# Performance work log

Hardware: AMD Instinct MI355X
Metric: run time of the kernel (lower is better)

## Reference

```python
import jax, jax.numpy as jnp
import numpy as np

B = 128      # batch
L = 28       # seq len (MNIST rows)
F = 28       # input feature (MNIST cols)
DM = 256     # d_model
EXPAND = 2
DI = EXPAND * DM   # d_inner = 512
DS = 16      # d_state
DR = DM // 16      # dt_rank = 16
K = 3        # d_conv
NL = 5       # n_layers
OUT = 10     # output_size


def setup_inputs() -> dict:
    key = jax.random.key(0)
    ks = jax.random.split(key, 12)
    s = 0.02
    x = jax.random.normal(ks[0], (B, 1, L, F), jnp.float32)
    input_proj_w = jax.random.normal(ks[1], (DM, F), jnp.float32) * s
    in_proj_w = jax.random.normal(ks[2], (NL, 2 * DI, DM), jnp.float32) * s
    conv_w = jax.random.normal(ks[3], (NL, DI, K), jnp.float32) * s
    conv_b = jnp.zeros((NL, DI), jnp.float32)
    x_proj_w = jax.random.normal(ks[4], (NL, DR + 2 * DS, DI), jnp.float32) * s
    dt_proj_w = jax.random.normal(ks[5], (NL, DI, DR), jnp.float32) * s
    dt_proj_b = jnp.full((NL, DI), -4.0, jnp.float32)  # softplus -> small dt
    # S4D-real init: A = -[1..d_state]
    A_log = jnp.log(jnp.broadcast_to(jnp.arange(1, DS + 1, dtype=jnp.float32), (NL, DI, DS)))
    D = jnp.ones((NL, DI), jnp.float32)
    out_proj_w = jax.random.normal(ks[6], (NL, DM, DI), jnp.float32) * s
    classifier_w = jax.random.normal(ks[7], (OUT, DM), jnp.float32) * s
    return {"x": x, "input_proj_w": input_proj_w, "in_proj_w": in_proj_w,
            "conv_w": conv_w, "conv_b": conv_b, "x_proj_w": x_proj_w,
            "dt_proj_w": dt_proj_w, "dt_proj_b": dt_proj_b, "A_log": A_log,
            "D": D, "out_proj_w": out_proj_w, "classifier_w": classifier_w}


def mamba_block(h, in_w, cw, cb, xw, dtw, dtb, A_log, D_vec, ow):
    # h: (B, L, DM)
    xz = h @ in_w.T                      # (B, L, 2*DI)
    xb, z = jnp.split(xz, 2, axis=-1)    # each (B, L, DI)
    # causal depthwise conv over time
    xc = xb.transpose(0, 2, 1)           # (B, DI, L)
    xc = jax.lax.conv_general_dilated(
        xc, cw[:, None, :], window_strides=(1,), padding=[(K - 1, 0)],
        dimension_numbers=("NCH", "OIH", "NCH"), feature_group_count=DI)
    xc = xc + cb[None, :, None]
    u = jax.nn.silu(xc.transpose(0, 2, 1))          # (B, L, DI)
    dbc = u @ xw.T                                   # (B, L, DR+2*DS)
    dt, Bm, Cm = dbc[..., :DR], dbc[..., DR:DR + DS], dbc[..., DR + DS:]
    delta = jax.nn.softplus(dt @ dtw.T + dtb)        # (B, L, DI)
    A = -jnp.exp(A_log)                              # (DI, DS)

    def step(hst, t):
        u_t, d_t, b_t, c_t = t                       # (B,DI),(B,DI),(B,DS),(B,DS)
        hst = jnp.exp(d_t[..., None] * A) * hst + (d_t * u_t)[..., None] * b_t[:, None, :]
        y = jnp.einsum("bds,bs->bd", hst, c_t)
        return hst, y

    h0 = jnp.zeros((u.shape[0], DI, DS), u.dtype)
    xs = (u.transpose(1, 0, 2), delta.transpose(1, 0, 2),
          Bm.transpose(1, 0, 2), Cm.transpose(1, 0, 2))
    _, ys = jax.lax.scan(step, h0, xs)               # (L, B, DI)
    y = ys.transpose(1, 0, 2) + u * D_vec            # skip term D*u
    y = y * jax.nn.silu(z)
    return y @ ow.T                                  # (B, L, DM)


def reference(x, input_proj_w, in_proj_w, conv_w, conv_b, x_proj_w,
              dt_proj_w, dt_proj_b, A_log, D, out_proj_w, classifier_w):
    h = x[:, 0] @ input_proj_w.T                     # squeeze(1), (B, L, DM)
    for i in range(NL):
        h = h + mamba_block(h, in_proj_w[i], conv_w[i], conv_b[i], x_proj_w[i],
                            dt_proj_w[i], dt_proj_b[i], A_log[i], D[i], out_proj_w[i])
    pooled = h.mean(axis=1)                          # (B, DM)
    return pooled @ classifier_w.T                   # (B, OUT)
```

## Files before the change

kernel.cpp:

```cpp
#include <hip/hip_runtime.h>
#include <hip/hip_bf16.h>
#include <cstdint>

#define BB 128
#define LL 28
#define FF 28
#define DM 256
#define DI 512
#define DS 16
#define DR 16
#define KK 3
#define NLAYER 5
#define NOUT 10
#define NTOK (BB * LL)
#define NDBC (DR + 2 * DS)

#define N_INW (NLAYER * 2 * DI * DM)
#define N_OPW (NLAYER * DM * DI)
#define N_XPW (NLAYER * NDBC * DI)
#define CAST_BLOCKS ((N_INW + N_OPW + N_XPW) / 1024)
#define INPROJ_BLOCKS ((DM / 64) * (NTOK / 64))

typedef __attribute__((ext_vector_type(8))) short bf16x8;
typedef __attribute__((ext_vector_type(4))) float f32x4;

__device__ __forceinline__ float sigmoidf_(float x) { return 1.0f / (1.0f + __expf(-x)); }
__device__ __forceinline__ float siluf_(float x) { return x * sigmoidf_(x); }
__device__ __forceinline__ float softplus_fast(float x) {
    return (x > 20.0f) ? x : __logf(1.0f + __expf(x));
}

__global__ __launch_bounds__(256) void k_prep(
        const float* __restrict__ inw, const float* __restrict__ opw,
        const float* __restrict__ xpw,
        __hip_bfloat16* __restrict__ inwb, __hip_bfloat16* __restrict__ opwb,
        __hip_bfloat16* __restrict__ xpwb,
        const float* __restrict__ x, const float* __restrict__ ipw,
        float* __restrict__ h, __hip_bfloat16* __restrict__ hb) {
    const int bid = blockIdx.x;
    if (bid < CAST_BLOCKS) {
        int i = (bid * 256 + threadIdx.x) * 4;
        const float* s; __hip_bfloat16* d; int off;
        if (i < N_INW) { s = inw; d = inwb; off = i; }
        else if (i < N_INW + N_OPW) { s = opw; d = opwb; off = i - N_INW; }
        else if (i < N_INW + N_OPW + N_XPW) { s = xpw; d = xpwb; off = i - N_INW - N_OPW; }
        else return;
        float4 v = *(const float4*)&s[off];
        d[off + 0] = __float2bfloat16(v.x);
        d[off + 1] = __float2bfloat16(v.y);
        d[off + 2] = __float2bfloat16(v.z);
        d[off + 3] = __float2bfloat16(v.w);
    } else {
        constexpr int K = FF, N = DM;
        __shared__ float As[16][68];
        __shared__ float Ws[16][68];
        const int b2 = bid - CAST_BLOCKS;
        const int bm = (b2 >> 2) * 64;
        const int bn = (b2 & 3) * 64;
        const int tid = threadIdx.x;
        const int kk = tid & 15, row = tid >> 4;
        const int tx = tid & 15, ty = tid >> 4;
        float acc[4][4];
        #pragma unroll
        for (int i = 0; i < 4; ++i)
            #pragma unroll
            for (int j = 0; j < 4; ++j) acc[i][j] = 0.f;
        for (int k0 = 0; k0 < K; k0 += 16) {
            const int k = k0 + kk;
            const bool kok = (k < K);
            #pragma unroll
            for (int r = 0; r < 4; ++r) {
                As[kk][r * 16 + row] = kok ? x[(size_t)(bm + r * 16 + row) * K + k] : 0.f;
                Ws[kk][r * 16 + row] = kok ? ipw[(size_t)(bn + r * 16 + row) * K + k] : 0.f;
            }
            __syncthreads();
            #pragma unroll
            for (int k2 = 0; k2 < 16; ++k2) {
                float a[4], b[4];
                #pragma unroll
                for (int i = 0; i < 4; ++i) a[i] = As[k2][ty * 4 + i];
                #pragma unroll
                for (int j = 0; j < 4; ++j) b[j] = Ws[k2][tx * 4 + j];
                #pragma unroll
                for (int i = 0; i < 4; ++i)
                    #pragma unroll
                    for (int j = 0; j < 4; ++j) acc[i][j] += a[i] * b[j];
            }
            __syncthreads();
        }
        #pragma unroll
        for (int i = 0; i < 4; ++i) {
            const int m = bm + ty * 4 + i;
            #pragma unroll
            for (int j = 0; j < 4; ++j) {
                const int n = bn + tx * 4 + j;
                float v = acc[i][j];
                h[(size_t)m * N + n] = v;
                hb[(size_t)m * N + n] = __float2bfloat16(v);
            }
        }
    }
}

__global__ __launch_bounds__(256) void k_xz_conv(
        const __hip_bfloat16* __restrict__ hb,
        const __hip_bfloat16* __restrict__ inw_l,
        const float* __restrict__ convw_l,
        const float* __restrict__ convb_l,
        __hip_bfloat16* __restrict__ ub,
        __hip_bfloat16* __restrict__ gzb) {
    __shared__ __align__(16) __hip_bfloat16 As[32][264];
    __shared__ __align__(16) __hip_bfloat16 Ws[64][264];
    __shared__ __align__(16) __hip_bfloat16 xbt[32][72];

    const int b = blockIdx.y;
    const int n0 = blockIdx.x * 64;
    const int t = threadIdx.x;
    const int wave = t >> 6, lane = t & 63;
    const int rla = lane & 15, koff = (lane >> 4) * 8;
    const int lrow = (lane >> 4) * 4, lcol = lane & 15;

    for (int i = t; i < 28 * 32; i += 256) {
        const int r = i >> 5, c = (i & 31) * 8;
        *(int4*)&As[r][c] = *(const int4*)&hb[(size_t)(b * LL + r) * DM + c];
    }
    for (int i = t; i < 64 * 32; i += 256) {
        const int r = i >> 5, c = (i & 31) * 8;
        *(int4*)&Ws[r][c] = *(const int4*)&inw_l[(size_t)(n0 + r) * DM + c];
    }
    __syncthreads();

    f32x4 acc0 = {}, acc1 = {};
    #pragma unroll
    for (int ks = 0; ks < 8; ++ks) {
        bf16x8 bf = *(const bf16x8*)&Ws[wave * 16 + rla][ks * 32 + koff];
        bf16x8 a0 = *(const bf16x8*)&As[rla][ks * 32 + koff];
        bf16x8 a1 = *(const bf16x8*)&As[16 + rla][ks * 32 + koff];
        acc0 = __builtin_amdgcn_mfma_f32_16x16x32_bf16(a0, bf, acc0, 0, 0, 0);
        acc1 = __builtin_amdgcn_mfma_f32_16x16x32_bf16(a1, bf, acc1, 0, 0, 0);
    }

    const int ncol = wave * 16 + lcol;
    if (n0 < DI) {
        #pragma unroll
        for (int r = 0; r < 4; ++r) {
            const int m0 = lrow + r, m1 = 16 + lrow + r;
            xbt[m0][ncol] = __float2bfloat16(acc0[r]);
            if (m1 < LL) xbt[m1][ncol] = __float2bfloat16(acc1[r]);
        }
        __syncthreads();
        const int col = t & 63, lg = t >> 6;
        const int di = n0 + col;
        const float c0 = convw_l[di * KK + 0];
        const float c1 = convw_l[di * KK + 1];
        const float c2 = convw_l[di * KK + 2];
        const float cbv = convb_l[di];
        const int l0 = lg * 7;
        float xm2 = (l0 >= 2) ? __bfloat162float(xbt[l0 - 2][col]) : 0.f;
        float xm1 = (l0 >= 1) ? __bfloat162float(xbt[l0 - 1][col]) : 0.f;
        #pragma unroll
        for (int j = 0; j < 7; ++j) {
            const int l = l0 + j;
            const float x0 = __bfloat162float(xbt[l][col]);
            const float v = siluf_(cbv + c0 * xm2 + c1 * xm1 + c2 * x0);
            xm2 = xm1; xm1 = x0;
            ub[(size_t)(b * LL + l) * DI + di] = __float2bfloat16(v);
        }
    } else {
        const int zc = n0 - DI + ncol;
        #pragma unroll
        for (int r = 0; r < 4; ++r) {
            const int m0 = lrow + r, m1 = 16 + lrow + r;
            gzb[(size_t)(b * LL + m0) * DI + zc] = __float2bfloat16(siluf_(acc0[r]));
            if (m1 < LL)
                gzb[(size_t)(b * LL + m1) * DI + zc] = __float2bfloat16(siluf_(acc1[r]));
        }
    }
}

__global__ __launch_bounds__(256) void k_xproj(
        const __hip_bfloat16* __restrict__ ub,
        const __hip_bfloat16* __restrict__ xpw_l,
        float* __restrict__ dbc) {
    __shared__ __align__(16) __hip_bfloat16 As[32][520];

    const int m0 = blockIdx.x * 32;
    const int t = threadIdx.x;
    const int wave = t >> 6, lane = t & 63;
    const int rla = lane & 15, koff = (lane >> 4) * 8;
    const int lrow = (lane >> 4) * 4, lcol = lane & 15;

    for (int i = t; i < 32 * 64; i += 256) {
        const int r = i >> 6, c = (i & 63) * 8;
        *(int4*)&As[r][c] = *(const int4*)&ub[(size_t)(m0 + r) * DI + c];
    }
    __syncthreads();

    #pragma unroll
    for (int cc = 0; cc < 2; ++cc) {
        const int c = wave + cc * 4;
        if (c < 6) {
            const int mt = c & 1, nt = c >> 1;
            f32x4 acc = {};
            #pragma unroll
            for (int ks = 0; ks < 16; ++ks) {
                bf16x8 bf = *(const bf16x8*)&xpw_l[(size_t)(nt * 16 + rla) * DI + ks * 32 + koff];
                bf16x8 af = *(const bf16x8*)&As[mt * 16 + rla][ks * 32 + koff];
                acc = __builtin_amdgcn_mfma_f32_16x16x32_bf16(af, bf, acc, 0, 0, 0);
            }
            #pragma unroll
            for (int r = 0; r < 4; ++r)
                dbc[(size_t)(m0 + mt * 16 + lrow + r) * NDBC + nt * 16 + lcol] = acc[r];
        }
    }
}

__global__ __launch_bounds__(256) void k_scan(
        const __hip_bfloat16* __restrict__ ub,
        const __hip_bfloat16* __restrict__ gzb,
        const float* __restrict__ dbc,
        const float* __restrict__ dtw_l,
        const float* __restrict__ dtb_l,
        const float* __restrict__ alog_l,
        const float* __restrict__ Dvec_l,
        __hip_bfloat16* __restrict__ yb) {
    __shared__ __align__(16) __hip_bfloat16 sus[LL][64];
    __shared__ __align__(16) __hip_bfloat16 sgz[LL][64];
    __shared__ float sdbc[LL][NDBC];
    __shared__ float sdelta[LL][64];
    __shared__ __align__(16) __hip_bfloat16 sy[LL][64];

    const int b = blockIdx.x;
    const int cg = blockIdx.y;
    const int di0 = cg * 64;
    const int t = threadIdx.x;
    const int wave = t >> 6, lane = t & 63;

    for (int i = t; i < 224; i += 256) {
        const int r = i >> 3, c = (i & 7) * 8;
        *(int4*)&sus[r][c] = *(const int4*)&ub[(size_t)(b * LL + r) * DI + di0 + c];
        *(int4*)&sgz[r][c] = *(const int4*)&gzb[(size_t)(b * LL + r) * DI + di0 + c];
    }
    {
        const float4* s4 = (const float4*)(dbc + (size_t)b * LL * NDBC);
        float4* d4 = (float4*)&sdbc[0][0];
        for (int i = t; i < LL * NDBC / 4; i += 256) d4[i] = s4[i];
    }

    float wrow[DR];
    {
        const float4* w4 = (const float4*)(dtw_l + (size_t)(di0 + lane) * DR);
        #pragma unroll
        for (int q = 0; q < DR / 4; ++q) {
            float4 v = w4[q];
            wrow[q * 4 + 0] = v.x; wrow[q * 4 + 1] = v.y;
            wrow[q * 4 + 2] = v.z; wrow[q * 4 + 3] = v.w;
        }
    }
    const float dbias = dtb_l[di0 + lane];
    __syncthreads();

    #pragma unroll
    for (int j = 0; j < 7; ++j) {
        const int l = wave * 7 + j;
        const float4 q0 = *(const float4*)&sdbc[l][0];
        const float4 q1 = *(const float4*)&sdbc[l][4];
        const float4 q2 = *(const float4*)&sdbc[l][8];
        const float4 q3 = *(const float4*)&sdbc[l][12];
        float d0 = wrow[0] * q0.x + wrow[1] * q0.y + wrow[2] * q0.z + wrow[3] * q0.w;
        float d1 = wrow[4] * q1.x + wrow[5] * q1.y + wrow[6] * q1.z + wrow[7] * q1.w;
        float d2 = wrow[8] * q2.x + wrow[9] * q2.y + wrow[10] * q2.z + wrow[11] * q2.w;
        float d3 = wrow[12] * q3.x + wrow[13] * q3.y + wrow[14] * q3.z + wrow[15] * q3.w;
        sdelta[l][lane] = softplus_fast(((d0 + d1) + (d2 + d3)) + dbias);
    }

    const int c = t >> 2, sq = t & 3;
    const int di = di0 + c;
    float4 aq = *(const float4*)&alog_l[(size_t)di * DS + sq * 4];
    const float A0 = -__expf(aq.x), A1 = -__expf(aq.y);
    const float A2 = -__expf(aq.z), A3 = -__expf(aq.w);
    const float Dd = Dvec_l[di];

    __syncthreads();

    float st0 = 0.f, st1 = 0.f, st2 = 0.f, st3 = 0.f;
    #pragma unroll 2
    for (int l = 0; l < LL; ++l) {
        const float d = sdelta[l][c];
        const float uu = __bfloat162float(sus[l][c]);
        const float du = d * uu;
        const float4 Bq = *(const float4*)&sdbc[l][DR + sq * 4];
        const float4 Cq = *(const float4*)&sdbc[l][DR + DS + sq * 4];
        st0 = __expf(d * A0) * st0 + du * Bq.x;
        st1 = __expf(d * A1) * st1 + du * Bq.y;
        st2 = __expf(d * A2) * st2 + du * Bq.z;
        st3 = __expf(d * A3) * st3 + du * Bq.w;
        float yp = st0 * Cq.x + st1 * Cq.y + st2 * Cq.z + st3 * Cq.w;
        yp += __shfl_xor(yp, 1);
        yp += __shfl_xor(yp, 2);
        if (sq == 0) {
            const float g = __bfloat162float(sgz[l][c]);
            sy[l][c] = __float2bfloat16((yp + uu * Dd) * g);
        }
    }
    __syncthreads();

    for (int i = t; i < 224; i += 256) {
        const int r = i >> 3, cc = (i & 7) * 8;
        *(int4*)&yb[(size_t)(b * LL + r) * DI + di0 + cc] = *(const int4*)&sy[r][cc];
    }
}

template <int LAST>
__global__ __launch_bounds__(256) void k_outproj(
        const __hip_bfloat16* __restrict__ yb,
        const __hip_bfloat16* __restrict__ opw_l,
        float* __restrict__ h,
        __hip_bfloat16* __restrict__ hb,
        const float* __restrict__ clsw,
        float* __restrict__ out) {
    __shared__ __align__(16) __hip_bfloat16 As[32][520];

    const int b = blockIdx.y;
    const int n0 = blockIdx.x * 32;
    const int t = threadIdx.x;
    const int wave = t >> 6, lane = t & 63;
    const int rla = lane & 15, koff = (lane >> 4) * 8;
    const int lrow = (lane >> 4) * 4, lcol = lane & 15;

    for (int i = t; i < 28 * 64; i += 256) {
        const int r = i >> 6, c = (i & 63) * 8;
        *(int4*)&As[r][c] = *(const int4*)&yb[(size_t)(b * LL + r) * DI + c];
    }
    __syncthreads();

    const int mt = wave & 1, nt = wave >> 1;
    f32x4 acc = {};
    #pragma unroll
    for (int ks = 0; ks < 16; ++ks) {
        bf16x8 bf = *(const bf16x8*)&opw_l[(size_t)(n0 + nt * 16 + rla) * DI + ks * 32 + koff];
        bf16x8 af = *(const bf16x8*)&As[mt * 16 + rla][ks * 32 + koff];
        acc = __builtin_amdgcn_mfma_f32_16x16x32_bf16(af, bf, acc, 0, 0, 0);
    }
    #pragma unroll
    for (int r = 0; r < 4; ++r) {
        const int m = mt * 16 + lrow + r;
        if (m < LL) {
            const int n = n0 + nt * 16 + lcol;
            const size_t idx = (size_t)(b * LL + m) * DM + n;
            const float v = h[idx] + acc[r];
            h[idx] = v;
            hb[idx] = __float2bfloat16(v);
        }
    }

    if (LAST) {
        __shared__ float pooled[32];
        __syncthreads();
        if (t < 32) {
            float p = 0.f;
            for (int l = 0; l < LL; ++l) p += h[(size_t)(b * LL + l) * DM + n0 + t];
            pooled[t] = p * (1.0f / LL);
        }
        __syncthreads();
        if (t < NOUT) {
            const float* cw = clsw + t * DM + n0;
            float a0 = 0.f, a1 = 0.f, a2 = 0.f, a3 = 0.f;
            #pragma unroll
            for (int n = 0; n < 32; n += 4) {
                a0 += pooled[n + 0] * cw[n + 0];
                a1 += pooled[n + 1] * cw[n + 1];
                a2 += pooled[n + 2] * cw[n + 2];
                a3 += pooled[n + 3] * cw[n + 3];
            }
            atomicAdd(&out[b * NOUT + t], (a0 + a1) + (a2 + a3));
        }
    }
}

extern "C" void kernel_launch(void* const* d_in, const int* in_sizes, int n_in,
                              void* d_out, int out_size, void* d_ws, size_t ws_size,
                              hipStream_t stream) {
    const float* x       = (const float*)d_in[0];
    const float* ipw     = (const float*)d_in[1];
    const float* inw     = (const float*)d_in[2];
    const float* convw   = (const float*)d_in[3];
    const float* convb   = (const float*)d_in[4];
    const float* xpw     = (const float*)d_in[5];
    const float* dtw     = (const float*)d_in[6];
    const float* dtb     = (const float*)d_in[7];
    const float* alog    = (const float*)d_in[8];
    const float* Dvec    = (const float*)d_in[9];
    const float* opw     = (const float*)d_in[10];
    const float* clsw    = (const float*)d_in[11];
    float* out = (float*)d_out;

    float* h   = (float*)d_ws;
    float* dbc = h + (size_t)NTOK * DM;
    __hip_bfloat16* hb   = (__hip_bfloat16*)(dbc + (size_t)NTOK * NDBC);
    __hip_bfloat16* ub   = hb + (size_t)NTOK * DM;
    __hip_bfloat16* gzb  = ub + (size_t)NTOK * DI;
    __hip_bfloat16* yb   = gzb + (size_t)NTOK * DI;
    __hip_bfloat16* inwb = yb + (size_t)NTOK * DI;
    __hip_bfloat16* opwb = inwb + N_INW;
    __hip_bfloat16* xpwb = opwb + N_OPW;

    hipMemsetAsync(out, 0, (size_t)BB * NOUT * sizeof(float), stream);

    hipLaunchKernelGGL(k_prep, dim3(CAST_BLOCKS + INPROJ_BLOCKS), dim3(256), 0, stream,
                       inw, opw, xpw, inwb, opwb, xpwb, x, ipw, h, hb);

    for (int layer = 0; layer < NLAYER; ++layer) {
        const __hip_bfloat16* inwb_l = inwb + (size_t)layer * 2 * DI * DM;
        const __hip_bfloat16* xpwb_l = xpwb + (size_t)layer * NDBC * DI;
        const __hip_bfloat16* opwb_l = opwb + (size_t)layer * DM * DI;
        const float* convw_l = convw + (size_t)layer * DI * KK;
        const float* convb_l = convb + (size_t)layer * DI;
        const float* dtw_l   = dtw  + (size_t)layer * DI * DR;
        const float* dtb_l   = dtb  + (size_t)layer * DI;
        const float* alog_l  = alog + (size_t)layer * DI * DS;
        const float* Dvec_l  = Dvec + (size_t)layer * DI;

        hipLaunchKernelGGL(k_xz_conv, dim3(16, BB), dim3(256), 0, stream,
                           hb, inwb_l, convw_l, convb_l, ub, gzb);

        hipLaunchKernelGGL(k_xproj, dim3(NTOK / 32), dim3(256), 0, stream,
                           ub, xpwb_l, dbc);

        hipLaunchKernelGGL(k_scan, dim3(BB, 8), dim3(256), 0, stream,
                           ub, gzb, dbc, dtw_l, dtb_l, alog_l, Dvec_l, yb);

        if (layer < NLAYER - 1) {
            hipLaunchKernelGGL((k_outproj<0>), dim3(8, BB), dim3(256), 0, stream,
                               yb, opwb_l, h, hb, clsw, out);
        } else {
            hipLaunchKernelGGL((k_outproj<1>), dim3(8, BB), dim3(256), 0, stream,
                               yb, opwb_l, h, hb, clsw, out);
        }
    }
}
```

Measured before the change: 280.5 us.

## Fuse x_proj GEMM into the selective scan kernel

Removes the separate k_xproj launch and its global dbc buffer. Each scan block now loads the full 28x512 u tile for its batch into LDS and computes the dt/B/C projection with MFMA directly into shared memory. It then reuses that same LDS tile to stage the gated output. This saves one kernel launch per layer and a global write/read of dbc. In exchange, the x_proj GEMM is recomputed redundantly by each of the 8 channel-group blocks per batch, and the larger LDS footprint may reduce occupancy.

```diff
diff --git a/kernel.cpp b/kernel.cpp
--- a/kernel.cpp
+++ b/kernel.cpp
@@ -178,22 +178,48 @@
     }
 }
 
-__global__ __launch_bounds__(256) void k_xproj(
+__global__ __launch_bounds__(256) void k_scan_fx(
         const __hip_bfloat16* __restrict__ ub,
+        const __hip_bfloat16* __restrict__ gzb,
         const __hip_bfloat16* __restrict__ xpw_l,
-        float* __restrict__ dbc) {
-    __shared__ __align__(16) __hip_bfloat16 As[32][520];
-
-    const int m0 = blockIdx.x * 32;
+        const float* __restrict__ dtw_l,
+        const float* __restrict__ dtb_l,
+        const float* __restrict__ alog_l,
+        const float* __restrict__ Dvec_l,
+        __hip_bfloat16* __restrict__ yb) {
+    __shared__ __align__(16) __hip_bfloat16 Us[32][520];
+    __shared__ __align__(16) __hip_bfloat16 sgz[LL][64];
+    __shared__ float sdbc[LL][NDBC];
+    __shared__ float sdelta[LL][64];
+
+    const int b = blockIdx.x;
+    const int cg = blockIdx.y;
+    const int di0 = cg * 64;
     const int t = threadIdx.x;
     const int wave = t >> 6, lane = t & 63;
     const int rla = lane & 15, koff = (lane >> 4) * 8;
     const int lrow = (lane >> 4) * 4, lcol = lane & 15;
 
-    for (int i = t; i < 32 * 64; i += 256) {
+    for (int i = t; i < 28 * 64; i += 256) {
         const int r = i >> 6, c = (i & 63) * 8;
-        *(int4*)&As[r][c] = *(const int4*)&ub[(size_t)(m0 + r) * DI + c];
-    }
+        *(int4*)&Us[r][c] = *(const int4*)&ub[(size_t)(b * LL + r) * DI + c];
+    }
+    for (int i = t; i < 224; i += 256) {
+        const int r = i >> 3, c = (i & 7) * 8;
+        *(int4*)&sgz[r][c] = *(const int4*)&gzb[(size_t)(b * LL + r) * DI + di0 + c];
+    }
+
+    float wrow[DR];
+    {
+        const float4* w4 = (const float4*)(dtw_l + (size_t)(di0 + lane) * DR);
+        #pragma unroll
+        for (int q = 0; q < DR / 4; ++q) {
+            float4 v = w4[q];
+            wrow[q * 4 + 0] = v.x; wrow[q * 4 + 1] = v.y;
+            wrow[q * 4 + 2] = v.z; wrow[q * 4 + 3] = v.w;
+        }
+    }
+    const float dbias = dtb_l[di0 + lane];
     __syncthreads();
 
     #pragma unroll
@@ -205,59 +231,16 @@
             #pragma unroll
             for (int ks = 0; ks < 16; ++ks) {
                 bf16x8 bf = *(const bf16x8*)&xpw_l[(size_t)(nt * 16 + rla) * DI + ks * 32 + koff];
-                bf16x8 af = *(const bf16x8*)&As[mt * 16 + rla][ks * 32 + koff];
+                bf16x8 af = *(const bf16x8*)&Us[mt * 16 + rla][ks * 32 + koff];
                 acc = __builtin_amdgcn_mfma_f32_16x16x32_bf16(af, bf, acc, 0, 0, 0);
             }
             #pragma unroll
-            for (int r = 0; r < 4; ++r)
-                dbc[(size_t)(m0 + mt * 16 + lrow + r) * NDBC + nt * 16 + lcol] = acc[r];
-        }
-    }
-}
-
-__global__ __launch_bounds__(256) void k_scan(
-        const __hip_bfloat16* __restrict__ ub,
-        const __hip_bfloat16* __restrict__ gzb,
-        const float* __restrict__ dbc,
-        const float* __restrict__ dtw_l,
-        const float* __restrict__ dtb_l,
-        const float* __restrict__ alog_l,
-        const float* __restrict__ Dvec_l,
-        __hip_bfloat16* __restrict__ yb) {
-    __shared__ __align__(16) __hip_bfloat16 sus[LL][64];
-    __shared__ __align__(16) __hip_bfloat16 sgz[LL][64];
-    __shared__ float sdbc[LL][NDBC];
-    __shared__ float sdelta[LL][64];
-    __shared__ __align__(16) __hip_bfloat16 sy[LL][64];
-
-    const int b = blockIdx.x;
-    const int cg = blockIdx.y;
-    const int di0 = cg * 64;
-    const int t = threadIdx.x;
-    const int wave = t >> 6, lane = t & 63;
-
-    for (int i = t; i < 224; i += 256) {
-        const int r = i >> 3, c = (i & 7) * 8;
-        *(int4*)&sus[r][c] = *(const int4*)&ub[(size_t)(b * LL + r) * DI + di0 + c];
-        *(int4*)&sgz[r][c] = *(const int4*)&gzb[(size_t)(b * LL + r) * DI + di0 + c];
-    }
-    {
-        const float4* s4 = (const float4*)(dbc + (size_t)b * LL * NDBC);
-        float4* d4 = (float4*)&sdbc[0][0];
-        for (int i = t; i < LL * NDBC / 4; i += 256) d4[i] = s4[i];
-    }
-
-    float wrow[DR];
-    {
-        const float4* w4 = (const float4*)(dtw_l + (size_t)(di0 + lane) * DR);
-        #pragma unroll
-        for (int q = 0; q < DR / 4; ++q) {
-            float4 v = w4[q];
-            wrow[q * 4 + 0] = v.x; wrow[q * 4 + 1] = v.y;
-            wrow[q * 4 + 2] = v.z; wrow[q * 4 + 3] = v.w;
-        }
-    }
-    const float dbias = dtb_l[di0 + lane];
+            for (int r = 0; r < 4; ++r) {
+                const int m = mt * 16 + lrow + r;
+                if (m < LL) sdbc[m][nt * 16 + lcol] = acc[r];
+            }
+        }
+    }
     __syncthreads();
 
     #pragma unroll
@@ -287,7 +270,7 @@
     #pragma unroll 2
     for (int l = 0; l < LL; ++l) {
         const float d = sdelta[l][c];
-        const float uu = __bfloat162float(sus[l][c]);
+        const float uu = __bfloat162float(Us[l][di0 + c]);
         const float du = d * uu;
         const float4 Bq = *(const float4*)&sdbc[l][DR + sq * 4];
         const float4 Cq = *(const float4*)&sdbc[l][DR + DS + sq * 4];
@@ -300,14 +283,14 @@
         yp += __shfl_xor(yp, 2);
         if (sq == 0) {
             const float g = __bfloat162float(sgz[l][c]);
-            sy[l][c] = __float2bfloat16((yp + uu * Dd) * g);
+            Us[l][di0 + c] = __float2bfloat16((yp + uu * Dd) * g);
         }
     }
     __syncthreads();
 
     for (int i = t; i < 224; i += 256) {
-        const int r = i >> 3, cc = (i & 7) * 8;
-        *(int4*)&yb[(size_t)(b * LL + r) * DI + di0 + cc] = *(const int4*)&sy[r][cc];
+        const int r = i >> 3, cc2 = (i & 7) * 8;
+        *(int4*)&yb[(size_t)(b * LL + r) * DI + di0 + cc2] = *(const int4*)&Us[r][di0 + cc2];
     }
 }
 
@@ -395,9 +378,8 @@
     const float* clsw    = (const float*)d_in[11];
     float* out = (float*)d_out;
 
-    float* h   = (float*)d_ws;
-    float* dbc = h + (size_t)NTOK * DM;
-    __hip_bfloat16* hb   = (__hip_bfloat16*)(dbc + (size_t)NTOK * NDBC);
+    float* h = (float*)d_ws;
+    __hip_bfloat16* hb   = (__hip_bfloat16*)(h + (size_t)NTOK * DM);
     __hip_bfloat16* ub   = hb + (size_t)NTOK * DM;
     __hip_bfloat16* gzb  = ub + (size_t)NTOK * DI;
     __hip_bfloat16* yb   = gzb + (size_t)NTOK * DI;
@@ -424,11 +406,8 @@
         hipLaunchKernelGGL(k_xz_conv, dim3(16, BB), dim3(256), 0, stream,
                            hb, inwb_l, convw_l, convb_l, ub, gzb);
 
-        hipLaunchKernelGGL(k_xproj, dim3(NTOK / 32), dim3(256), 0, stream,
-                           ub, xpwb_l, dbc);
-
-        hipLaunchKernelGGL(k_scan, dim3(BB, 8), dim3(256), 0, stream,
-                           ub, gzb, dbc, dtw_l, dtb_l, alog_l, Dvec_l, yb);
+        hipLaunchKernelGGL(k_scan_fx, dim3(BB, 8), dim3(256), 0, stream,
+                           ub, gzb, xpwb_l, dtw_l, dtb_l, alog_l, Dvec_l, yb);
 
         if (layer < NLAYER - 1) {
             hipLaunchKernelGGL((k_outproj<0>), dim3(8, BB), dim3(256), 0, stream,
```

Result: slower. 319.6 us (+14.0%).
